# Optimization experiments

Hardware: AMD Instinct MI355X
Metric: run time of the kernel (lower is better)

## Reference

```python
import jax, jax.numpy as jnp
import numpy as np

DIM = 384
NUM_HEADS = 12
WIN = 7
N = WIN * WIN  # 49
B = 4096


def _relative_position_index():
    coords = np.stack(np.meshgrid(np.arange(WIN), np.arange(WIN), indexing='ij'))  # (2,W,W)
    cf = coords.reshape(2, -1)  # (2, N)
    rel = cf[:, :, None] - cf[:, None, :]  # (2, N, N)
    rel = rel.transpose(1, 2, 0).astype(np.int64)  # (N, N, 2)
    rel[:, :, 0] += WIN - 1
    rel[:, :, 1] += WIN - 1
    rel[:, :, 0] *= 2 * WIN - 1
    return jnp.asarray(rel.sum(-1), dtype=jnp.int32)  # (N, N)


def setup_inputs() -> dict:
    key = jax.random.key(0)
    ks = jax.random.split(key, 6)
    x = jax.random.normal(ks[0], (B, N, DIM), dtype=jnp.float32)
    mask = jnp.zeros((B, N, N), dtype=jnp.float32)
    qkv_w = jax.random.normal(ks[1], (3 * DIM, DIM), dtype=jnp.float32) * 0.02
    qkv_b = jnp.zeros((3 * DIM,), dtype=jnp.float32)
    proj_w = jax.random.normal(ks[2], (DIM, DIM), dtype=jnp.float32) * 0.02
    proj_b = jnp.zeros((DIM,), dtype=jnp.float32)
    bias_table = jax.random.normal(ks[3], ((2 * WIN - 1) ** 2, NUM_HEADS), dtype=jnp.float32) * 0.02
    rel_index = _relative_position_index()
    return {"x": x, "mask": mask, "qkv_w": qkv_w, "qkv_b": qkv_b,
            "proj_w": proj_w, "proj_b": proj_b, "bias_table": bias_table,
            "rel_index": rel_index}


def reference(x, mask, qkv_w, qkv_b, proj_w, proj_b, bias_table, rel_index):
    B_, n, C = x.shape
    H = NUM_HEADS
    d = C // H
    scale = d ** (-0.5)
    # fused qkv projection: (B_, n, 3, H, d)
    qkv = (x @ qkv_w.T + qkv_b).reshape(B_, n, 3, H, d)
    qkv = jnp.transpose(qkv, (2, 0, 3, 1, 4))  # (3, B_, H, n, d)
    q, k, v = qkv[0], qkv[1], qkv[2]
    attn = jnp.einsum('bhnd,bhmd->bhnm', q * scale, k)  # (B_, H, n, n)
    # relative position bias gather: (n, n, H) -> (H, n, n)
    rel_bias = jnp.transpose(bias_table[rel_index], (2, 0, 1))
    attn = attn + rel_bias[None] + mask[:, None]
    attn = jax.nn.softmax(attn, axis=-1)
    out = jnp.einsum('bhnm,bhmd->bnhd', attn, v).reshape(B_, n, C)
    return out @ proj_w.T + proj_b
```

## Files before the change

kernel.cpp:

```cpp
#include <hip/hip_runtime.h>
#include <hip/hip_bf16.h>

#define NWIN   4096
#define NTOK   49
#define CDIM   384
#define NHEAD  12
#define QKVN   1152

typedef __attribute__((ext_vector_type(8))) short bf16x8;
typedef __attribute__((ext_vector_type(4))) float f32x4;
typedef unsigned int u32;
typedef unsigned short u16;

static __device__ __forceinline__ float bf2f(u16 v) {
  union { u32 u; float f; } w; w.u = ((u32)v) << 16; return w.f;
}
static __device__ __forceinline__ u16 f2bf(float f) {
  union { float f; u32 u; } w; w.f = f;
  u32 r = w.u + 0x7fffu + ((w.u >> 16) & 1u);
  return (u16)(r >> 16);
}
static __device__ __forceinline__ float blo(u32 v) {
  union { u32 u; float f; } w; w.u = v << 16; return w.f;
}
static __device__ __forceinline__ float bhi(u32 v) {
  union { u32 u; float f; } w; w.u = v & 0xffff0000u; return w.f;
}
static __device__ __forceinline__ void gld_lds16(const u16* g, u16* l) {
  __builtin_amdgcn_global_load_lds((const __attribute__((address_space(1))) u32*)g,
                                   (__attribute__((address_space(3))) u32*)l, 16, 0, 0);
}

__global__ void k_prep(const float* __restrict__ qkv_w, const float* __restrict__ proj_w,
                       const float* __restrict__ btab, const int* __restrict__ ridx,
                       u16* __restrict__ wq, u16* __restrict__ wp, u32* __restrict__ rbp)
{
  const int n1 = QKVN * CDIM;
  const int n2 = CDIM * CDIM;
  const int n3 = NHEAD * NTOK * 26;
  for (int i = blockIdx.x * blockDim.x + threadIdx.x; i < n1 + n2 + n3;
       i += gridDim.x * blockDim.x) {
    if (i < n1) {
      wq[i] = f2bf(qkv_w[i]);
    } else if (i < n1 + n2) {
      wp[i - n1] = f2bf(proj_w[i - n1]);
    } else {
      int t = i - n1 - n2;
      int h = t / (NTOK * 26); int rem = t % (NTOK * 26);
      int r = rem / 26, p = rem % 26;
      float lo = 0.f, hi = 0.f;
      if (p < 25) {
        lo = btab[ridx[r * NTOK + 2 * p] * NHEAD + h];
        if (2 * p + 1 < NTOK) hi = btab[ridx[r * NTOK + 2 * p + 1] * NHEAD + h];
      }
      rbp[(h * NTOK + r) * 26 + p] = (u32)f2bf(lo) | ((u32)f2bf(hi) << 16);
    }
  }
}

__global__ void k_convx(const float* __restrict__ x, u16* __restrict__ xb, long n8)
{
  long i = (long)blockIdx.x * blockDim.x + threadIdx.x;
  long stride = (long)gridDim.x * blockDim.x;
  for (; i < n8; i += stride) {
    const float4* p = (const float4*)x + i * 2;
    float4 a = p[0], b = p[1];
    u32 w0 = (u32)f2bf(a.x) | ((u32)f2bf(a.y) << 16);
    u32 w1 = (u32)f2bf(a.z) | ((u32)f2bf(a.w) << 16);
    u32 w2 = (u32)f2bf(b.x) | ((u32)f2bf(b.y) << 16);
    u32 w3 = (u32)f2bf(b.z) | ((u32)f2bf(b.w) << 16);
    uint4 v; v.x = w0; v.y = w1; v.z = w2; v.w = w3;
    ((uint4*)xb)[i] = v;
  }
}

template<bool OUT_BF16>
__global__ __launch_bounds__(256, 2)
void k_gemm(const u16* __restrict__ A, int lda,
            const u16* __restrict__ Bt, const float* __restrict__ bias,
            void* __restrict__ C, int ldc, int K, int tiles_n)
{
  __shared__ alignas(16) u16 As[128 * 64];
  __shared__ alignas(16) u16 Bs[128 * 64];
  const int tid = threadIdx.x;
  const int w = tid >> 6, l = tid & 63;
  const int tm = blockIdx.x / tiles_n, tn = blockIdx.x % tiles_n;
  const int wm = (w >> 1) * 64, wn = (w & 1) * 64;
  const long arow0 = (long)tm * 128;
  const long brow0 = (long)tn * 128;
  const int r8 = l >> 3;
  const int c8 = (l & 7) * 8;

  f32x4 acc[4][4];
  const f32x4 z = {0.f, 0.f, 0.f, 0.f};
#pragma unroll
  for (int m = 0; m < 4; ++m)
#pragma unroll
    for (int n = 0; n < 4; ++n) acc[m][n] = z;

  for (int kk = 0; kk < K; kk += 64) {
    __syncthreads();
#pragma unroll
    for (int q = 0; q < 4; ++q) {
      int ra = w * 32 + q * 8;
      gld_lds16(A  + (arow0 + ra + r8) * (long)lda + kk + c8, &As[ra * 64]);
      gld_lds16(Bt + (brow0 + ra + r8) * (long)K   + kk + c8, &Bs[ra * 64]);
    }
    __syncthreads();
#pragma unroll
    for (int ks = 0; ks < 2; ++ks) {
      const int ko = ks * 32 + (l >> 4) * 8;
      const int rl = l & 15;
      bf16x8 af[4], bfr[4];
#pragma unroll
      for (int m = 0; m < 4; ++m) af[m]  = *(const bf16x8*)&As[(wm + m * 16 + rl) * 64 + ko];
#pragma unroll
      for (int n = 0; n < 4; ++n) bfr[n] = *(const bf16x8*)&Bs[(wn + n * 16 + rl) * 64 + ko];
#pragma unroll
      for (int m = 0; m < 4; ++m)
#pragma unroll
        for (int n = 0; n < 4; ++n)
          acc[m][n] = __builtin_amdgcn_mfma_f32_16x16x32_bf16(af[m], bfr[n], acc[m][n], 0, 0, 0);
    }
  }

  const int rl = l & 15, rh = (l >> 4) * 4;
  float bv[4];
#pragma unroll
  for (int n = 0; n < 4; ++n) bv[n] = bias[tn * 128 + wn + n * 16 + rl];
#pragma unroll
  for (int m = 0; m < 4; ++m) {
#pragma unroll
    for (int n = 0; n < 4; ++n) {
      const long col = brow0 + wn + n * 16 + rl;
#pragma unroll
      for (int j = 0; j < 4; ++j) {
        const long row = arow0 + wm + m * 16 + rh + j;
        float v = acc[m][n][j] + bv[n];
        if (OUT_BF16) ((u16*)C)[row * ldc + col] = f2bf(v);
        else          ((float*)C)[row * ldc + col] = v;
      }
    }
  }
}

__global__ __launch_bounds__(384, 2)
void k_attn(u16* __restrict__ qkv, const float* __restrict__ maskc,
            const u32* __restrict__ rbp)
{
  __shared__ alignas(16) u16 Vt[6][32 * 64];
  __shared__ alignas(16) u16 Pb[6][64 * 64];
  __shared__ alignas(16) u32 mp[NTOK * 26];
  const int tid = threadIdx.x;
  const int w = tid >> 6, l = tid & 63;
  const int g = l >> 4, li = l & 15;
  const int id = blockIdx.x;
  const int logical = (id & 7) * ((int)gridDim.x >> 3) + (id >> 3);
  const int bl = logical >> 1, hg = logical & 1;
  const int h = hg * 6 + w;
  const long rowbase = (long)bl * NTOK;
  const float scale = 0.17677669529663687f;

  u16* vt = Vt[w];
  {
    const int jj = l >> 2;
    const int d0 = (l & 3) * 8;
#pragma unroll
    for (int it = 0; it < 4; ++it) {
      int j = it * 16 + jj;
      bf16x8 vv = {0, 0, 0, 0, 0, 0, 0, 0};
      if (j < NTOK)
        vv = *(const bf16x8*)(qkv + (rowbase + j) * QKVN + 2 * CDIM + h * 32 + d0);
#pragma unroll
      for (int t = 0; t < 8; ++t)
        vt[(d0 + t) * 64 + (j ^ (t << 3))] = (u16)vv[t];
    }
  }
  for (int e = tid; e < NTOK * 25; e += 384) {
    int i = e / 25, p = e - i * 25;
    const float* mrow = maskc + (long)bl * (NTOK * NTOK) + i * NTOK;
    float lo = mrow[2 * p];
    float hi = (2 * p + 1 < NTOK) ? mrow[2 * p + 1] : 0.f;
    mp[i * 26 + p] = (u32)f2bf(lo) | ((u32)f2bf(hi) << 16);
  }
  if (tid < NTOK) mp[tid * 26 + 25] = 0;
  __syncthreads();

  bf16x8 kf[4], qf[4];
#pragma unroll
  for (int jm = 0; jm < 4; ++jm) {
    int rj = jm * 16 + li; if (rj >= NTOK) rj = NTOK - 1;
    kf[jm] = *(const bf16x8*)(qkv + (rowbase + rj) * QKVN + CDIM + h * 32 + g * 8);
  }
#pragma unroll
  for (int in = 0; in < 4; ++in) {
    int ri = in * 16 + li; if (ri >= NTOK) ri = NTOK - 1;
    qf[in] = *(const bf16x8*)(qkv + (rowbase + ri) * QKVN + h * 32 + g * 8);
  }
  const f32x4 z = {0.f, 0.f, 0.f, 0.f};
  f32x4 st[4][4];
#pragma unroll
  for (int jm = 0; jm < 4; ++jm)
#pragma unroll
    for (int in = 0; in < 4; ++in)
      st[jm][in] = __builtin_amdgcn_mfma_f32_16x16x32_bf16(kf[jm], qf[in], z, 0, 0, 0);

#pragma unroll
  for (int jm = 0; jm < 4; ++jm) {
    int p0 = 8 * jm + 2 * g; if (p0 > 24) p0 = 24;
#pragma unroll
    for (int in = 0; in < 4; ++in) {
      int i = 16 * in + li; int ic = i < NTOK ? i : NTOK - 1;
      const u32* bp = rbp + (h * NTOK + ic) * 26 + p0;
      u32 b0w = bp[0], b1w = bp[1];
      u32 m0w = mp[ic * 26 + p0], m1w = mp[ic * 26 + p0 + 1];
      st[jm][in][0] = st[jm][in][0] * scale + blo(b0w) + blo(m0w);
      st[jm][in][1] = st[jm][in][1] * scale + bhi(b0w) + bhi(m0w);
      st[jm][in][2] = st[jm][in][2] * scale + blo(b1w) + blo(m1w);
      st[jm][in][3] = st[jm][in][3] * scale + bhi(b1w) + bhi(m1w);
    }
  }

  float inv[4];
#pragma unroll
  for (int in = 0; in < 4; ++in) {
    float mx = -3.0e38f;
#pragma unroll
    for (int jm = 0; jm < 4; ++jm)
#pragma unroll
      for (int rr = 0; rr < 4; ++rr) mx = fmaxf(mx, st[jm][in][rr]);
    mx = fmaxf(mx, __shfl_xor(mx, 16));
    mx = fmaxf(mx, __shfl_xor(mx, 32));
    float sum = 0.f;
#pragma unroll
    for (int jm = 0; jm < 4; ++jm) {
      const int j0 = 16 * jm + 4 * g;
#pragma unroll
      for (int rr = 0; rr < 4; ++rr) {
        float p = (j0 + rr < NTOK) ? __expf(st[jm][in][rr] - mx) : 0.f;
        st[jm][in][rr] = p; sum += p;
      }
    }
    sum += __shfl_xor(sum, 16);
    sum += __shfl_xor(sum, 32);
    inv[in] = (16 * in + li < NTOK) ? (1.f / sum) : 0.f;
  }

  u16* pb = Pb[w];
  const int sw = (li & 7) << 3;
#pragma unroll
  for (int in = 0; in < 4; ++in) {
    const int i = 16 * in + li;
#pragma unroll
    for (int jm = 0; jm < 4; ++jm) {
      const int j0 = 16 * jm + 4 * g;
      u32 w0 = (u32)f2bf(st[jm][in][0] * inv[in]) | ((u32)f2bf(st[jm][in][1] * inv[in]) << 16);
      u32 w1 = (u32)f2bf(st[jm][in][2] * inv[in]) | ((u32)f2bf(st[jm][in][3] * inv[in]) << 16);
      const int base = i * 64 + (j0 ^ sw);
      *(u32*)&pb[base] = w0;
      *(u32*)&pb[base + 2] = w1;
    }
  }

  f32x4 oacc[4][2];
#pragma unroll
  for (int im = 0; im < 4; ++im)
#pragma unroll
    for (int dn = 0; dn < 2; ++dn) oacc[im][dn] = z;
#pragma unroll
  for (int ks = 0; ks < 2; ++ks) {
    const int jb = ks * 32 + g * 8;
    bf16x8 pf[4], vf[2];
#pragma unroll
    for (int im = 0; im < 4; ++im)
      pf[im] = *(const bf16x8*)&pb[(16 * im + li) * 64 + (jb ^ sw)];
#pragma unroll
    for (int dn = 0; dn < 2; ++dn)
      vf[dn] = *(const bf16x8*)&vt[(16 * dn + li) * 64 + (jb ^ sw)];
#pragma unroll
    for (int im = 0; im < 4; ++im)
#pragma unroll
      for (int dn = 0; dn < 2; ++dn)
        oacc[im][dn] = __builtin_amdgcn_mfma_f32_16x16x32_bf16(pf[im], vf[dn], oacc[im][dn], 0, 0, 0);
  }

#pragma unroll
  for (int im = 0; im < 4; ++im) {
#pragma unroll
    for (int rr = 0; rr < 4; ++rr) {
      const int i = 16 * im + 4 * g + rr;
      if (i < NTOK) {
        u16* orow = qkv + (rowbase + i) * QKVN + h * 32;
#pragma unroll
        for (int dn = 0; dn < 2; ++dn)
          orow[16 * dn + li] = f2bf(oacc[im][dn][rr]);
      }
    }
  }
}

extern "C" void kernel_launch(void* const* d_in, const int* in_sizes, int n_in,
                              void* d_out, int out_size, void* d_ws, size_t ws_size,
                              hipStream_t stream)
{
  const float* x      = (const float*)d_in[0];
  const float* mask   = (const float*)d_in[1];
  const float* qkv_w  = (const float*)d_in[2];
  const float* qkv_b  = (const float*)d_in[3];
  const float* proj_w = (const float*)d_in[4];
  const float* proj_b = (const float*)d_in[5];
  const float* btab   = (const float*)d_in[6];
  const int*   ridx   = (const int*)d_in[7];
  float* out = (float*)d_out;

  auto need = [](int bc) -> size_t {
    return (size_t)bc * NTOK * QKVN * 2
         + (size_t)bc * NTOK * CDIM * 2
         + (size_t)QKVN * CDIM * 2
         + (size_t)CDIM * CDIM * 2
         + (size_t)NHEAD * NTOK * 26 * 4
         + 1024;
  };
  int BC = NWIN;
  while (BC > 128 && need(BC) > ws_size) BC >>= 1;

  char* p = (char*)d_ws;
  u16* qkvbuf = (u16*)p;  p += (size_t)BC * NTOK * QKVN * 2;
  u16* xb     = (u16*)p;  p += (size_t)BC * NTOK * CDIM * 2;
  u16* wq     = (u16*)p;  p += (size_t)QKVN * CDIM * 2;
  u16* wp     = (u16*)p;  p += (size_t)CDIM * CDIM * 2;
  u32* rbp    = (u32*)p;

  k_prep<<<512, 256, 0, stream>>>(qkv_w, proj_w, btab, ridx, wq, wp, rbp);

  const int nc = NWIN / BC;
  const int Mc = BC * NTOK;
  for (int c = 0; c < nc; ++c) {
    const float* xc = x + (size_t)c * Mc * CDIM;
    k_convx<<<2048, 256, 0, stream>>>(xc, xb, (long)Mc * CDIM / 8);
    k_gemm<true><<<(Mc / 128) * 9, 256, 0, stream>>>(
        xb, CDIM, wq, qkv_b, (void*)qkvbuf, QKVN, CDIM, 9);
    k_attn<<<BC * 2, 384, 0, stream>>>(
        qkvbuf, mask + (size_t)c * BC * NTOK * NTOK, rbp);
    k_gemm<false><<<(Mc / 128) * 3, 256, 0, stream>>>(
        qkvbuf, QKVN, wp, proj_b, (void*)(out + (size_t)c * Mc * CDIM), CDIM, CDIM, 3);
  }
}
```

Before: 815.5 us.

## Feed softmax probabilities to PV MFMA from registers and vectorize GEMM epilogue

The attention kernel no longer writes the normalized probability tile to shared memory and reads it back. It packs the score accumulators straight into bf16 MFMA A-operands with v_cvt_pk_bf16_f32, and permutes the V k-index reads to match that register layout. This removes the per-wave 8KB LDS buffer and its round trip, which may also help occupancy. The GEMM swaps the MFMA operand order so each lane holds four consecutive output columns, allowing vectorized bias loads and packed 8- or 16-byte stores instead of scalar stores. The register-layout permutation must exactly match the V index mapping, so any mismatch would give wrong results.

Measured after the change: 797.6 us. -2.2%, faster.

```diff
diff --git a/kernel.cpp b/kernel.cpp
--- a/kernel.cpp
+++ b/kernel.cpp
@@ -8,13 +8,12 @@
 #define QKVN   1152
 
 typedef __attribute__((ext_vector_type(8))) short bf16x8;
+typedef __attribute__((ext_vector_type(4))) short bf16x4;
 typedef __attribute__((ext_vector_type(4))) float f32x4;
+typedef __attribute__((ext_vector_type(2))) unsigned int u32x2;
 typedef unsigned int u32;
 typedef unsigned short u16;
 
-static __device__ __forceinline__ float bf2f(u16 v) {
-  union { u32 u; float f; } w; w.u = ((u32)v) << 16; return w.f;
-}
 static __device__ __forceinline__ u16 f2bf(float f) {
   union { float f; u32 u; } w; w.f = f;
   u32 r = w.u + 0x7fffu + ((w.u >> 16) & 1u);
@@ -25,6 +24,10 @@
 }
 static __device__ __forceinline__ float bhi(u32 v) {
   union { u32 u; float f; } w; w.u = v & 0xffff0000u; return w.f;
+}
+static __device__ __forceinline__ u32 cvtpk2(float lo, float hi) {
+  u32 r; asm("v_cvt_pk_bf16_f32 %0, %1, %2" : "=v"(r) : "v"(lo), "v"(hi));
+  return r;
 }
 static __device__ __forceinline__ void gld_lds16(const u16* g, u16* l) {
   __builtin_amdgcn_global_load_lds((const __attribute__((address_space(1))) u32*)g,
@@ -120,25 +123,33 @@
       for (int m = 0; m < 4; ++m)
 #pragma unroll
         for (int n = 0; n < 4; ++n)
-          acc[m][n] = __builtin_amdgcn_mfma_f32_16x16x32_bf16(af[m], bfr[n], acc[m][n], 0, 0, 0);
-    }
-  }
-
-  const int rl = l & 15, rh = (l >> 4) * 4;
-  float bv[4];
-#pragma unroll
-  for (int n = 0; n < 4; ++n) bv[n] = bias[tn * 128 + wn + n * 16 + rl];
+          acc[m][n] = __builtin_amdgcn_mfma_f32_16x16x32_bf16(bfr[n], af[m], acc[m][n], 0, 0, 0);
+    }
+  }
+
+  const int li = l & 15, g4 = (l >> 4) * 4;
+  float4 bv[4];
+#pragma unroll
+  for (int n = 0; n < 4; ++n)
+    bv[n] = *(const float4*)&bias[tn * 128 + wn + n * 16 + g4];
 #pragma unroll
   for (int m = 0; m < 4; ++m) {
+    const long row = arow0 + wm + m * 16 + li;
 #pragma unroll
     for (int n = 0; n < 4; ++n) {
-      const long col = brow0 + wn + n * 16 + rl;
-#pragma unroll
-      for (int j = 0; j < 4; ++j) {
-        const long row = arow0 + wm + m * 16 + rh + j;
-        float v = acc[m][n][j] + bv[n];
-        if (OUT_BF16) ((u16*)C)[row * ldc + col] = f2bf(v);
-        else          ((float*)C)[row * ldc + col] = v;
+      const long colb = brow0 + wn + n * 16 + g4;
+      float v0 = acc[m][n][0] + bv[n].x;
+      float v1 = acc[m][n][1] + bv[n].y;
+      float v2 = acc[m][n][2] + bv[n].z;
+      float v3 = acc[m][n][3] + bv[n].w;
+      if (OUT_BF16) {
+        u32x2 pk;
+        pk[0] = (u32)f2bf(v0) | ((u32)f2bf(v1) << 16);
+        pk[1] = (u32)f2bf(v2) | ((u32)f2bf(v3) << 16);
+        *(u32x2*)((u16*)C + row * ldc + colb) = pk;
+      } else {
+        float4 pk; pk.x = v0; pk.y = v1; pk.z = v2; pk.w = v3;
+        *(float4*)((float*)C + row * ldc + colb) = pk;
       }
     }
   }
@@ -149,7 +160,6 @@
             const u32* __restrict__ rbp)
 {
   __shared__ alignas(16) u16 Vt[6][32 * 64];
-  __shared__ alignas(16) u16 Pb[6][64 * 64];
   __shared__ alignas(16) u32 mp[NTOK * 26];
   const int tid = threadIdx.x;
   const int w = tid >> 6, l = tid & 63;
@@ -246,42 +256,32 @@
     inv[in] = (16 * in + li < NTOK) ? (1.f / sum) : 0.f;
   }
 
-  u16* pb = Pb[w];
+  f32x4 oacc[4][2];
+#pragma unroll
+  for (int im = 0; im < 4; ++im)
+#pragma unroll
+    for (int dn = 0; dn < 2; ++dn) oacc[im][dn] = z;
   const int sw = (li & 7) << 3;
 #pragma unroll
-  for (int in = 0; in < 4; ++in) {
-    const int i = 16 * in + li;
-#pragma unroll
-    for (int jm = 0; jm < 4; ++jm) {
-      const int j0 = 16 * jm + 4 * g;
-      u32 w0 = (u32)f2bf(st[jm][in][0] * inv[in]) | ((u32)f2bf(st[jm][in][1] * inv[in]) << 16);
-      u32 w1 = (u32)f2bf(st[jm][in][2] * inv[in]) | ((u32)f2bf(st[jm][in][3] * inv[in]) << 16);
-      const int base = i * 64 + (j0 ^ sw);
-      *(u32*)&pb[base] = w0;
-      *(u32*)&pb[base + 2] = w1;
-    }
-  }
-
-  f32x4 oacc[4][2];
-#pragma unroll
-  for (int im = 0; im < 4; ++im)
-#pragma unroll
-    for (int dn = 0; dn < 2; ++dn) oacc[im][dn] = z;
-#pragma unroll
   for (int ks = 0; ks < 2; ++ks) {
-    const int jb = ks * 32 + g * 8;
-    bf16x8 pf[4], vf[2];
-#pragma unroll
-    for (int im = 0; im < 4; ++im)
-      pf[im] = *(const bf16x8*)&pb[(16 * im + li) * 64 + (jb ^ sw)];
-#pragma unroll
-    for (int dn = 0; dn < 2; ++dn)
-      vf[dn] = *(const bf16x8*)&vt[(16 * dn + li) * 64 + (jb ^ sw)];
-#pragma unroll
-    for (int im = 0; im < 4; ++im)
+    union { bf16x4 h[2]; bf16x8 v8; } vf[2];
+#pragma unroll
+    for (int dn = 0; dn < 2; ++dn) {
+      const u16* vrow = &vt[(16 * dn + li) * 64];
+      vf[dn].h[0] = *(const bf16x4*)&vrow[(32 * ks + 4 * g) ^ sw];
+      vf[dn].h[1] = *(const bf16x4*)&vrow[(32 * ks + 16 + 4 * g) ^ sw];
+    }
+#pragma unroll
+    for (int im = 0; im < 4; ++im) {
+      union { u32 w[4]; bf16x8 v8; } pa;
+      pa.w[0] = cvtpk2(st[2 * ks][im][0] * inv[im], st[2 * ks][im][1] * inv[im]);
+      pa.w[1] = cvtpk2(st[2 * ks][im][2] * inv[im], st[2 * ks][im][3] * inv[im]);
+      pa.w[2] = cvtpk2(st[2 * ks + 1][im][0] * inv[im], st[2 * ks + 1][im][1] * inv[im]);
+      pa.w[3] = cvtpk2(st[2 * ks + 1][im][2] * inv[im], st[2 * ks + 1][im][3] * inv[im]);
 #pragma unroll
       for (int dn = 0; dn < 2; ++dn)
-        oacc[im][dn] = __builtin_amdgcn_mfma_f32_16x16x32_bf16(pf[im], vf[dn], oacc[im][dn], 0, 0, 0);
+        oacc[im][dn] = __builtin_amdgcn_mfma_f32_16x16x32_bf16(pa.v8, vf[dn].v8, oacc[im][dn], 0, 0, 0);
+    }
   }
 
 #pragma unroll
```
